# Performance work log

Hardware: AMD Instinct MI355X
Metric: run time of the kernel (lower is better)

## Reference

```python
import jax, jax.numpy as jnp
import numpy as np

BETA = 0.05
ALPHA = 0.01
CROSSCAM_EPOCH = 5
BG_KNN = 50
C, L, D = 8, 4096, 2048   # cameras, pseudo-classes per camera, feature dim
B = 256                   # batch, cam-sorted blocks of PERCAM samples
PERCAM = B // C


def setup_inputs() -> dict:
    key = jax.random.key(0)
    kf, km = jax.random.split(key)
    features = jax.random.normal(kf, (B, D), dtype=jnp.float32)
    # cams sorted in blocks; per-camera targets unique (PK-sampler style), spread over [0, L)
    cams = jnp.repeat(jnp.arange(C, dtype=jnp.int32), PERCAM)
    targets = jnp.tile(jnp.arange(PERCAM, dtype=jnp.int32) * (L // PERCAM), C)
    # dataset-level arrays: every camera observes all L labels -> identity class mapper,
    # concate_intra_class == tile(arange(L), C)
    all_img_cams = jnp.repeat(jnp.arange(C, dtype=jnp.int32), L)
    all_pseudo_label = jnp.tile(jnp.arange(L, dtype=jnp.int32), C)
    mem = jax.random.normal(km, (C, L, D), dtype=jnp.float32)
    init_intra_id_feat = mem / jnp.linalg.norm(mem, axis=-1, keepdims=True)
    return {"features": features, "targets": targets, "cams": cams,
            "all_pseudo_label": all_pseudo_label, "all_img_cams": all_img_cams,
            "init_intra_id_feat": init_intra_id_feat, "epoch": 10, "batch_ind": 0}


def _forward(features, init_intra_id_feat, targets, cams, epoch):
    Cn, Ln, Dn = init_intra_id_feat.shape
    Bn = features.shape[0]
    percam = Bn // Cn
    mem0 = jax.lax.stop_gradient(init_intra_id_feat)  # proxy memory buffer (detached in torch)
    # --- EMA memory update (torch.no_grad); (cam, target) pairs unique in batch ---
    f_sg = jax.lax.stop_gradient(features)
    old = mem0[cams, targets]                                   # [B, D] gather
    new = ALPHA * old + (1.0 - ALPHA) * f_sg
    new = new / jnp.linalg.norm(new, axis=1, keepdims=True)
    mem = mem0.at[cams, targets].set(new)                       # scatter update
    # --- per-camera proxy cross-entropy (cams are sorted blocks of `percam`) ---
    fn = features / jnp.linalg.norm(features, axis=1, keepdims=True)
    memn = mem / jnp.linalg.norm(mem, axis=-1, keepdims=True)   # rows already unit; faithful
    logits = jnp.einsum('cbd,cld->cbl', fn.reshape(Cn, percam, Dn), memn) / BETA
    lsm = jax.nn.log_softmax(logits, axis=-1)
    t = targets.reshape(Cn, percam)
    ce = -jnp.take_along_axis(lsm, t[..., None], axis=-1)[..., 0]   # [C, percam]
    loss = ce.mean(axis=1).sum()   # torch sums per-camera mean CE over unique batch cams
    # --- cross-camera associative loss (all_cam_feats built from pre-update memory) ---
    if epoch >= CROSSCAM_EPOCH:
        allf = mem0.reshape(Cn * Ln, Dn)
        allf = allf / jnp.linalg.norm(allf, axis=1, keepdims=True)
        sims = fn @ allf.T                                      # [B, C*L]
        # ori_asso_ind: label t appears once per camera block in concate_intra_class
        pos = targets[:, None] + jnp.arange(Cn)[None, :] * Ln   # [B, C]
        rows = jnp.arange(Bn)[:, None]
        pos_logits = sims[rows, pos] / BETA                     # [B, C]
        masked = sims.at[rows, pos].set(-10000.0)               # temp_sims masking
        topv, _ = jax.lax.top_k(masked, BG_KNN)                 # hardest negatives
        cat = jnp.concatenate([pos_logits, topv / BETA], axis=1)  # [B, C+BG_KNN]
        ls2 = jax.nn.log_softmax(cat, axis=1)
        per = -ls2[:, :Cn].sum(axis=1) / Cn                     # soft target 1/|ori| on positives
        loss = loss + 0.5 * per.reshape(Cn, percam).mean(axis=1).sum()
    return loss.reshape(1)


def reference(features, targets, cams, all_pseudo_label, all_img_cams,
              init_intra_id_feat, epoch, batch_ind):
    # all_pseudo_label / all_img_cams determine concate_intra_class; by construction
    # each camera holds all L labels, so positive indices are computed analytically.
    return _forward(features, init_intra_id_feat, targets, cams, epoch)
```

## Files before the change

kernel.cpp:

```cpp
#include <hip/hip_runtime.h>
#include <hip/hip_bf16.h>


#define Dn 2048
#define Ln 4096
#define Cn 8
#define Bn 256
#define NTOT 32768
#define INVB 20.0f
#define KNN 50

typedef __attribute__((ext_vector_type(8))) short short8;
typedef __attribute__((ext_vector_type(4))) float f32x4;

__device__ __forceinline__ unsigned short f2b(float f) {
    unsigned u = __float_as_uint(f);
    unsigned r = (u + 0x7FFFu + ((u >> 16) & 1u)) >> 16;
    return (unsigned short)r;
}

__device__ __forceinline__ unsigned pack2(float x, float y) {
    __hip_bfloat162 h = __float22bfloat162_rn(float2{x, y});
    unsigned u; __builtin_memcpy(&u, &h, 4); return u;
}

__device__ __forceinline__ unsigned fenc(float f) {
    unsigned u = __float_as_uint(f);
    return u ^ (((unsigned)((int)u >> 31)) | 0x80000000u);
}
__device__ __forceinline__ float fdec(unsigned e) {
    unsigned mask = (e & 0x80000000u) ? 0x80000000u : 0xFFFFFFFFu;
    return __uint_as_float(e ^ mask);
}

__global__ __launch_bounds__(256) void prep_kernel(
    const float* __restrict__ feat, const float* __restrict__ mem0,
    const int* __restrict__ targets, const int* __restrict__ cams,
    unsigned short* __restrict__ fnb, float* __restrict__ sdot,
    unsigned* __restrict__ rowmax, unsigned* __restrict__ rowmin) {
    __shared__ float red[2][4];
    __shared__ float lf[Dn];
    __shared__ float lnr[Dn];
    int i = blockIdx.x, tid = threadIdx.x;
    int c = cams[i], t = targets[i];
    const float* f = feat + (size_t)i * Dn;
    const float* o = mem0 + ((size_t)c * Ln + t) * Dn;
    if (tid == 0) { rowmax[i] = 0u; rowmin[i] = 0xFFFFFFFFu; }
    float fv[8], nv[8];
    float s1 = 0.f, s2 = 0.f;
#pragma unroll
    for (int r = 0; r < 8; ++r) {
        int idx = tid + (r << 8);
        float a = f[idx], bb = o[idx];
        float n = 0.99f * a + 0.01f * bb;
        fv[r] = a; nv[r] = n;
        s1 += a * a; s2 += n * n;
    }
    for (int off = 32; off > 0; off >>= 1) {
        s1 += __shfl_down(s1, off);
        s2 += __shfl_down(s2, off);
    }
    int wv = tid >> 6;
    if ((tid & 63) == 0) { red[0][wv] = s1; red[1][wv] = s2; }
    __syncthreads();
    s1 = red[0][0] + red[0][1] + red[0][2] + red[0][3];
    s2 = red[1][0] + red[1][1] + red[1][2] + red[1][3];
    float r1 = 1.0f / sqrtf(s1), r2 = 1.0f / sqrtf(s2);
#pragma unroll
    for (int r = 0; r < 8; ++r) {
        int idx = tid + (r << 8);
        float a = fv[r] * r1;
        fnb[(size_t)i * Dn + idx] = f2b(a);
        lf[idx] = a;
        lnr[idx] = nv[r] * r2;
    }
    __syncthreads();
    if (tid < 64) {
        float d = 0.f;
#pragma unroll
        for (int r = 0; r < 32; ++r) d += lf[tid + (r << 6)] * lnr[tid + (r << 6)];
        for (int off = 32; off > 0; off >>= 1) d += __shfl_down(d, off);
        if (tid == 0) sdot[i] = d;
    }
}

#define GSTEP(KIT, CUR, NXT)                                                      \
  {                                                                               \
    if ((KIT) + 1 < 32) {                                                         \
      _Pragma("unroll") for (int mf = 0; mf < 4; ++mf)                            \
        _Pragma("unroll") for (int kb = 0; kb < 2; ++kb)                          \
          av[NXT][mf][kb] =                                                       \
            *(const short8*)&fnb[aoff[mf] + ((KIT) + 1) * 64 + kb * 32];          \
    }                                                                             \
    if ((KIT) + 2 < 32) {                                                         \
      _Pragma("unroll") for (int r = 0; r < 4; ++r)                               \
        rb[CUR][r] = *(const float4*)&mem0[boff[r] + ((KIT) + 2) * 64];           \
    }                                                                             \
    _Pragma("unroll") for (int kb = 0; kb < 2; ++kb) {                            \
      short8 bv[4];                                                               \
      _Pragma("unroll") for (int nf = 0; nf < 4; ++nf)                            \
        bv[nf] = *(const short8*)&lB[CUR][(nf * 16 + fr) * 72 + kb * 32 + fg * 8];\
      _Pragma("unroll") for (int mf = 0; mf < 4; ++mf)                            \
        _Pragma("unroll") for (int nf = 0; nf < 4; ++nf)                          \
          acc[mf][nf] = __builtin_amdgcn_mfma_f32_16x16x32_bf16(                  \
              av[CUR][mf][kb], bv[nf], acc[mf][nf], 0, 0, 0);                     \
    }                                                                             \
    if ((KIT) + 1 < 32) {                                                         \
      _Pragma("unroll") for (int r = 0; r < 4; ++r) {                             \
        float4 v = rb[NXT][r];                                                    \
        uint2 h; h.x = pack2(v.x, v.y); h.y = pack2(v.z, v.w);                    \
        *(uint2*)&lB[NXT][(r * 16 + btr) * 72 + btc * 4] = h;                     \
      }                                                                           \
    }                                                                             \
    __syncthreads();                                                              \
  }

__global__ __launch_bounds__(256, 2) void gemm_sims(
    const float* __restrict__ mem0, const unsigned short* __restrict__ fnb,
    float* __restrict__ sims, unsigned* __restrict__ rowmax,
    unsigned* __restrict__ rowmin) {
    __shared__ __align__(16) unsigned short lB[2][64 * 72];
    int tid = threadIdx.x;
    int n0 = blockIdx.x * 64;
    int lane = tid & 63, wv = tid >> 6;
    int fr = lane & 15, fg = lane >> 4;
    int btr = tid >> 4, btc = tid & 15;

    f32x4 acc[4][4];
#pragma unroll
    for (int a = 0; a < 4; ++a)
#pragma unroll
        for (int b = 0; b < 4; ++b)
#pragma unroll
            for (int k = 0; k < 4; ++k) acc[a][b][k] = 0.0f;

    size_t aoff[4], boff[4];
#pragma unroll
    for (int mf = 0; mf < 4; ++mf)
        aoff[mf] = (size_t)(wv * 64 + mf * 16 + fr) * Dn + fg * 8;
#pragma unroll
    for (int r = 0; r < 4; ++r)
        boff[r] = (size_t)(n0 + r * 16 + btr) * Dn + btc * 4;

    float4 rb[2][4];
    short8 av[2][4][2];
#pragma unroll
    for (int r = 0; r < 4; ++r) rb[0][r] = *(const float4*)&mem0[boff[r]];
#pragma unroll
    for (int r = 0; r < 4; ++r) rb[1][r] = *(const float4*)&mem0[boff[r] + 64];
#pragma unroll
    for (int mf = 0; mf < 4; ++mf)
#pragma unroll
        for (int kb = 0; kb < 2; ++kb)
            av[0][mf][kb] = *(const short8*)&fnb[aoff[mf] + kb * 32];
#pragma unroll
    for (int r = 0; r < 4; ++r) {
        float4 v = rb[0][r];
        uint2 h; h.x = pack2(v.x, v.y); h.y = pack2(v.z, v.w);
        *(uint2*)&lB[0][(r * 16 + btr) * 72 + btc * 4] = h;
    }
    __syncthreads();

    for (int k2 = 0; k2 < 16; ++k2) {
        GSTEP(2 * k2, 0, 1);
        GSTEP(2 * k2 + 1, 1, 0);
    }

    float* tbuf = (float*)lB;
    int row16 = lane & 15, seg = lane >> 4;
#pragma unroll
    for (int mf = 0; mf < 4; ++mf) {
#pragma unroll
        for (int nf = 0; nf < 4; ++nf)
#pragma unroll
            for (int r = 0; r < 4; ++r)
                tbuf[wv * 1088 + (fg * 4 + r) * 68 + nf * 16 + fr] = acc[mf][nf][r];
        __syncthreads();
        float mx = -3e38f, mn = 3e38f;
        int m = wv * 64 + mf * 16 + row16;
#pragma unroll
        for (int q = 0; q < 4; ++q) {
            float4 v = *(float4*)&tbuf[wv * 1088 + row16 * 68 + seg * 16 + q * 4];
            *(float4*)&sims[(size_t)m * NTOT + n0 + seg * 16 + q * 4] = v;
            mx = fmaxf(fmaxf(mx, fmaxf(v.x, v.y)), fmaxf(v.z, v.w));
            mn = fminf(fminf(mn, fminf(v.x, v.y)), fminf(v.z, v.w));
        }
        mx = fmaxf(mx, __shfl_xor(mx, 16));
        mx = fmaxf(mx, __shfl_xor(mx, 32));
        mn = fminf(mn, __shfl_xor(mn, 16));
        mn = fminf(mn, __shfl_xor(mn, 32));
        if (seg == 0) {
            atomicMax(&rowmax[m], fenc(mx));
            atomicMin(&rowmin[m], fenc(mn));
        }
        __syncthreads();
    }
}

__global__ __launch_bounds__(256) void fused_kernel(
    const float* __restrict__ sims, const float* __restrict__ sdot,
    const int* __restrict__ targets, const unsigned* __restrict__ rowmax,
    const unsigned* __restrict__ rowmin, float* __restrict__ out) {
    __shared__ int hist[4][1024];
    __shared__ int ghist[64];
    __shared__ float buf[512];
    __shared__ int cnt, sh_bstar, sh_r, sh_total;
    __shared__ float wred[4], cesum[4];
    int i = blockIdx.x, tid = threadIdx.x;
    int wv = tid >> 6, lane = tid & 63;
    int t = targets[i], c = i >> 5;
    const float* row = sims + (size_t)i * NTOT;

    float hi = fdec(rowmax[i]);
    float lo = fdec(rowmin[i]);
    float rng = fmaxf(hi - lo, 1e-30f);

    float thr = 0.f, scale = 0.f;
    float ce_p = 0.f;
    for (int att = 0; att < 3; ++att) {
        float frac = (att == 0) ? 0.25f : ((att == 1) ? 0.5f : 1.0001f);
        thr = hi - rng * frac;
        scale = 1023.0f / fmaxf(hi - thr, 1e-30f);
        for (int k = tid; k < 4096; k += 256) ((int*)hist)[k] = 0;
        __syncthreads();
        for (int q = 0; q < 128; ++q) {
            int j = tid + (q << 8);
            float v = row[j];
            if (att == 0 && (j >> 12) == c) ce_p += expf(v * INVB);
            if (v > thr && (j & (Ln - 1)) != t) {
                int bin = min(1023, (int)((v - thr) * scale));
                atomicAdd(&hist[wv][bin], 1);
            }
        }
        __syncthreads();
        for (int k = tid; k < 1024; k += 256)
            hist[0][k] = hist[0][k] + hist[1][k] + hist[2][k] + hist[3][k];
        __syncthreads();
        if (tid < 64) {
            int s = 0;
#pragma unroll
            for (int k = 0; k < 16; ++k) s += hist[0][tid * 16 + k];
            ghist[tid] = s;
        }
        __syncthreads();
        if (tid == 0) {
            int total = 0;
            for (int g = 0; g < 64; ++g) total += ghist[g];
            sh_total = total;
            if (total >= KNN) {
                int cum = 0, g = 63;
                for (; g > 0; --g) { if (cum + ghist[g] >= KNN) break; cum += ghist[g]; }
                int bb = g * 16 + 15;
                for (;; --bb) { int h = hist[0][bb]; if (cum + h >= KNN) break; cum += h; }
                sh_bstar = bb;
                sh_r = KNN - cum;
            }
        }
        __syncthreads();
        if (sh_total >= KNN) break;
        __syncthreads();
    }
    for (int o = 32; o > 0; o >>= 1) ce_p += __shfl_down(ce_p, o);
    if (lane == 0) cesum[wv] = ce_p;
    int bstar = sh_bstar;
    if (tid == 0) cnt = 0;
    __syncthreads();
    float lsum = 0.f;
    for (int q = 0; q < 128; ++q) {
        int j = tid + (q << 8);
        float v = row[j];
        if (v <= thr || (j & (Ln - 1)) == t) continue;
        int bin = min(1023, (int)((v - thr) * scale));
        if (bin > bstar) {
            lsum += expf(v * INVB);
        } else if (bin == bstar) {
            int p = atomicAdd(&cnt, 1);
            if (p < 512) buf[p] = v;
        }
    }
    for (int o = 32; o > 0; o >>= 1) lsum += __shfl_down(lsum, o);
    if (lane == 0) wred[wv] = lsum;
    __syncthreads();
    if (wv == 0) {
        int nb = min(cnt, 512);
        int r = sh_r;
        float bsum = 0.f;
        for (int s = 0; s < r; ++s) {
            float mv = -3e38f; int mi = 0;
            for (int k = lane; k < nb; k += 64) {
                float v = buf[k];
                if (v > mv) { mv = v; mi = k; }
            }
            for (int o = 32; o > 0; o >>= 1) {
                float ov = __shfl_down(mv, o);
                int oi = __shfl_down(mi, o);
                if (ov > mv) { mv = ov; mi = oi; }
            }
            mi = __shfl(mi, 0); mv = __shfl(mv, 0);
            if (lane == 0) { buf[mi] = -3e38f; bsum += expf(mv * INVB); }
            __builtin_amdgcn_wave_barrier();
        }
        if (lane == 0) {
            float S = wred[0] + wred[1] + wred[2] + wred[3] + bsum;
            float psum = 0.f, pls = 0.f;
#pragma unroll
            for (int c2 = 0; c2 < Cn; ++c2) {
                float pv = row[t + c2 * Ln] * INVB;
                psum += expf(pv);
                pls += pv;
            }
            S += psum;
            float per = logf(S) - pls * (1.0f / Cn);
            float sd = sdot[i];
            float Sce = cesum[0] + cesum[1] + cesum[2] + cesum[3]
                        - expf(row[(c << 12) + t] * INVB) + expf(sd * INVB);
            float ce = logf(Sce) - sd * INVB;
            atomicAdd(out, ce * (1.0f / 32.0f) + 0.5f * per * (1.0f / 32.0f));
        }
    }
}

extern "C" void kernel_launch(void* const* d_in, const int* in_sizes, int n_in,
                              void* d_out, int out_size, void* d_ws, size_t ws_size,
                              hipStream_t stream) {
    const float* feat    = (const float*)d_in[0];
    const int*   targets = (const int*)d_in[1];
    const int*   cams    = (const int*)d_in[2];
    const float* mem0    = (const float*)d_in[5];
    float* out = (float*)d_out;
    char* ws = (char*)d_ws;
    unsigned short* fnb    = (unsigned short*)(ws);
    float*          sdot   = (float*)(ws + (size_t)(1 << 20));
    unsigned*       rowmax = (unsigned*)(ws + (size_t)(1 << 20) + 4096);
    unsigned*       rowmin = (unsigned*)(ws + (size_t)(1 << 20) + 8192);
    float*          sims   = (float*)(ws + (size_t)(8 << 20));

    hipMemsetAsync(d_out, 0, (size_t)out_size * sizeof(float), stream);
    prep_kernel<<<Bn, 256, 0, stream>>>(feat, mem0, targets, cams, fnb, sdot,
                                        rowmax, rowmin);
    gemm_sims<<<NTOT / 64, 256, 0, stream>>>(mem0, fnb, sims, rowmax, rowmin);
    fused_kernel<<<Bn, 256, 0, stream>>>(sims, sdot, targets, rowmax, rowmin, out);
}
```

Before: 488.6 us.

## Cache each sims row in registers with 1024-thread blocks and vector loads

After: 422.7 us. -13.5%, faster.

```diff
diff --git a/kernel.cpp b/kernel.cpp
--- a/kernel.cpp
+++ b/kernel.cpp
@@ -197,44 +197,71 @@
     }
 }
 
-__global__ __launch_bounds__(256) void fused_kernel(
+__global__ __launch_bounds__(1024) void fused_kernel(
     const float* __restrict__ sims, const float* __restrict__ sdot,
     const int* __restrict__ targets, const unsigned* __restrict__ rowmax,
     const unsigned* __restrict__ rowmin, float* __restrict__ out) {
-    __shared__ int hist[4][1024];
+    __shared__ int hist[8][1024];
     __shared__ int ghist[64];
     __shared__ float buf[512];
     __shared__ int cnt, sh_bstar, sh_r, sh_total;
-    __shared__ float wred[4], cesum[4];
+    __shared__ float wred[16], cesum[16];
     int i = blockIdx.x, tid = threadIdx.x;
     int wv = tid >> 6, lane = tid & 63;
     int t = targets[i], c = i >> 5;
     const float* row = sims + (size_t)i * NTOT;
+    const f32x4* row4 = (const f32x4*)row;
+
+    f32x4 f[8];
+#pragma unroll
+    for (int q = 0; q < 8; ++q) f[q] = row4[tid + (q << 10)];
+
+    if (tid == 0) cnt = 0;
+
+    int e0 = tid << 2;
+    bool m0 = (e0 + 0) != t, m1 = (e0 + 1) != t, m2 = (e0 + 2) != t, m3 = (e0 + 3) != t;
+
+    float ce_p = 0.f;
+#pragma unroll
+    for (int q = 0; q < 8; ++q) {
+        if (q == c) {
+            ce_p += expf(f[q][0] * INVB) + expf(f[q][1] * INVB)
+                  + expf(f[q][2] * INVB) + expf(f[q][3] * INVB);
+        }
+    }
+    for (int o = 32; o > 0; o >>= 1) ce_p += __shfl_down(ce_p, o);
+    if (lane == 0) cesum[wv] = ce_p;
 
     float hi = fdec(rowmax[i]);
     float lo = fdec(rowmin[i]);
     float rng = fmaxf(hi - lo, 1e-30f);
 
     float thr = 0.f, scale = 0.f;
-    float ce_p = 0.f;
     for (int att = 0; att < 3; ++att) {
         float frac = (att == 0) ? 0.25f : ((att == 1) ? 0.5f : 1.0001f);
         thr = hi - rng * frac;
         scale = 1023.0f / fmaxf(hi - thr, 1e-30f);
-        for (int k = tid; k < 4096; k += 256) ((int*)hist)[k] = 0;
-        __syncthreads();
-        for (int q = 0; q < 128; ++q) {
-            int j = tid + (q << 8);
-            float v = row[j];
-            if (att == 0 && (j >> 12) == c) ce_p += expf(v * INVB);
-            if (v > thr && (j & (Ln - 1)) != t) {
-                int bin = min(1023, (int)((v - thr) * scale));
-                atomicAdd(&hist[wv][bin], 1);
-            }
-        }
-        __syncthreads();
-        for (int k = tid; k < 1024; k += 256)
-            hist[0][k] = hist[0][k] + hist[1][k] + hist[2][k] + hist[3][k];
+        for (int k = tid; k < 8192; k += 1024) ((int*)hist)[k] = 0;
+        __syncthreads();
+        int hs = wv & 7;
+#pragma unroll
+        for (int q = 0; q < 8; ++q) {
+#pragma unroll
+            for (int e = 0; e < 4; ++e) {
+                float v = f[q][e];
+                bool ok = (e == 0) ? m0 : ((e == 1) ? m1 : ((e == 2) ? m2 : m3));
+                if (v > thr && ok) {
+                    int bin = min(1023, (int)((v - thr) * scale));
+                    atomicAdd(&hist[hs][bin], 1);
+                }
+            }
+        }
+        __syncthreads();
+        {
+            int s = hist[0][tid] + hist[1][tid] + hist[2][tid] + hist[3][tid]
+                  + hist[4][tid] + hist[5][tid] + hist[6][tid] + hist[7][tid];
+            hist[0][tid] = s;
+        }
         __syncthreads();
         if (tid < 64) {
             int s = 0;
@@ -260,22 +287,24 @@
         if (sh_total >= KNN) break;
         __syncthreads();
     }
-    for (int o = 32; o > 0; o >>= 1) ce_p += __shfl_down(ce_p, o);
-    if (lane == 0) cesum[wv] = ce_p;
     int bstar = sh_bstar;
-    if (tid == 0) cnt = 0;
-    __syncthreads();
+
     float lsum = 0.f;
-    for (int q = 0; q < 128; ++q) {
-        int j = tid + (q << 8);
-        float v = row[j];
-        if (v <= thr || (j & (Ln - 1)) == t) continue;
-        int bin = min(1023, (int)((v - thr) * scale));
-        if (bin > bstar) {
-            lsum += expf(v * INVB);
-        } else if (bin == bstar) {
-            int p = atomicAdd(&cnt, 1);
-            if (p < 512) buf[p] = v;
+#pragma unroll
+    for (int q = 0; q < 8; ++q) {
+#pragma unroll
+        for (int e = 0; e < 4; ++e) {
+            float v = f[q][e];
+            bool ok = (e == 0) ? m0 : ((e == 1) ? m1 : ((e == 2) ? m2 : m3));
+            if (v > thr && ok) {
+                int bin = min(1023, (int)((v - thr) * scale));
+                if (bin > bstar) {
+                    lsum += expf(v * INVB);
+                } else if (bin == bstar) {
+                    int p = atomicAdd(&cnt, 1);
+                    if (p < 512) buf[p] = v;
+                }
+            }
         }
     }
     for (int o = 32; o > 0; o >>= 1) lsum += __shfl_down(lsum, o);
@@ -301,7 +330,9 @@
             __builtin_amdgcn_wave_barrier();
         }
         if (lane == 0) {
-            float S = wred[0] + wred[1] + wred[2] + wred[3] + bsum;
+            float S = bsum;
+#pragma unroll
+            for (int w = 0; w < 16; ++w) S += wred[w];
             float psum = 0.f, pls = 0.f;
 #pragma unroll
             for (int c2 = 0; c2 < Cn; ++c2) {
@@ -312,8 +343,9 @@
             S += psum;
             float per = logf(S) - pls * (1.0f / Cn);
             float sd = sdot[i];
-            float Sce = cesum[0] + cesum[1] + cesum[2] + cesum[3]
-                        - expf(row[(c << 12) + t] * INVB) + expf(sd * INVB);
+            float Sce = -expf(row[(c << 12) + t] * INVB) + expf(sd * INVB);
+#pragma unroll
+            for (int w = 0; w < 16; ++w) Sce += cesum[w];
             float ce = logf(Sce) - sd * INVB;
             atomicAdd(out, ce * (1.0f / 32.0f) + 0.5f * per * (1.0f / 32.0f));
         }
@@ -339,5 +371,5 @@
     prep_kernel<<<Bn, 256, 0, stream>>>(feat, mem0, targets, cams, fnb, sdot,
                                         rowmax, rowmin);
     gemm_sims<<<NTOT / 64, 256, 0, stream>>>(mem0, fnb, sims, rowmax, rowmin);
-    fused_kernel<<<Bn, 256, 0, stream>>>(sims, sdot, targets, rowmax, rowmin, out);
-}
+    fused_kernel<<<Bn, 1024, 0, stream>>>(sims, sdot, targets, rowmax, rowmin, out);
+}
```
